# Kernel optimization log

Measured on AMD Instinct MI355X. Metric: run time of the kernel, lower is better.

The kernel has to match this reference:

```python
import jax, jax.numpy as jnp
import numpy as np

NODE_IN, EDGE_IN, HID, L = 16, 8, 128, 4
N_NODES, N_EDGES = 50000, 600000
EPS = 1e-5


def setup_inputs() -> dict:
    key = jax.random.key(0)
    ks = jax.random.split(key, 20)
    def lin(k, fan_in, fan_out):
        b = 1.0 / np.sqrt(fan_in)
        kw, kb = jax.random.split(k)
        return (jax.random.uniform(kw, (fan_in, fan_out), jnp.float32, -b, b),
                jax.random.uniform(kb, (fan_out,), jnp.float32, -b, b))
    x = jax.random.normal(ks[0], (N_NODES, NODE_IN), jnp.float32)
    edge_index = jax.random.randint(ks[1], (2, N_EDGES), 0, N_NODES, jnp.int64)
    edge_attr = jax.random.normal(ks[2], (N_EDGES, EDGE_IN), jnp.float32)
    node_w, node_b = lin(ks[3], NODE_IN, HID)
    edge_w, edge_b = lin(ks[4], EDGE_IN, HID)
    lnode_w, lnode_b, ledge_w, ledge_b, adm_w, adm_b = [], [], [], [], [], []
    for l in range(L):
        w, b = lin(ks[5 + 3 * l], HID, HID); lnode_w.append(w); lnode_b.append(b)
        w, b = lin(ks[6 + 3 * l], HID, HID); ledge_w.append(w); ledge_b.append(b)
        w, b = lin(ks[7 + 3 * l], HID, 1); adm_w.append(w); adm_b.append(b)
    return {
        "x": x, "edge_index": edge_index, "edge_attr": edge_attr,
        "node_w": node_w, "node_b": node_b, "edge_w": edge_w, "edge_b": edge_b,
        "lnode_w": jnp.stack(lnode_w), "lnode_b": jnp.stack(lnode_b),
        "ledge_w": jnp.stack(ledge_w), "ledge_b": jnp.stack(ledge_b),
        "adm_w": jnp.stack(adm_w), "adm_b": jnp.stack(adm_b),
        "gamma": jnp.ones((L, HID), jnp.float32),
        "beta": jnp.zeros((L, HID), jnp.float32),
    }


def reference(x, edge_index, edge_attr, node_w, node_b, edge_w, edge_b,
              lnode_w, lnode_b, ledge_w, ledge_b, adm_w, adm_b, gamma, beta):
    N = x.shape[0]
    src, dst = edge_index[0], edge_index[1]
    h = x @ node_w + node_b              # [N, HID]
    ea = edge_attr @ edge_w + edge_b     # [E, HID]
    for l in range(lnode_w.shape[0]):
        hn = h @ lnode_w[l] + lnode_b[l]                         # lin_node
        y_mag = jax.nn.sigmoid(ea @ adm_w[l] + adm_b[l])         # [E, 1] admittance gate
        e = ea @ ledge_w[l] + ledge_b[l]                         # lin_edge
        msg = y_mag * (hn[src] + e)                              # gated message [E, HID]
        agg = jax.ops.segment_sum(msg, dst, num_segments=N)      # scatter-add
        mu = jnp.mean(agg, axis=-1, keepdims=True)
        var = jnp.mean((agg - mu) ** 2, axis=-1, keepdims=True)
        xn = (agg - mu) * jax.lax.rsqrt(var + EPS) * gamma[l] + beta[l]
        h = h + jax.nn.relu(xn)          # dropout is identity in eval mode
    return h
```

## Files before the change

kernel.cpp:

```cpp
#include <hip/hip_runtime.h>
#include <math.h>

#define N_NODES 50000
#define N_EDGES 600000
#define HID 128
#define NLAYERS 4
#define NODE_IN 16
#define EDGE_IN 8
#define LN_EPS 1e-5f
#define SCAN_BLOCKS ((N_NODES + 255) / 256)

typedef short bf16x8 __attribute__((ext_vector_type(8)));
typedef float f32x4 __attribute__((ext_vector_type(4)));

__device__ __forceinline__ float b2f(unsigned short u) {
    union { unsigned int i; float f; } v; v.i = ((unsigned int)u) << 16; return v.f;
}
__device__ __forceinline__ unsigned short f2b(float x) {
    union { float f; unsigned int i; } v; v.f = x;
    unsigned int b = v.i + 0x7FFFu + ((v.i >> 16) & 1u);
    return (unsigned short)(b >> 16);
}

__global__ void detect_i64(const int* ei, int* flag) {
    __shared__ int nz;
    if (threadIdx.x == 0) nz = 0;
    __syncthreads();
    int acc = 0;
    for (int i = threadIdx.x; i < 1024; i += blockDim.x)
        if (ei[2 * i + 1] != 0) acc = 1;
    if (acc) atomicOr(&nz, 1);
    __syncthreads();
    if (threadIdx.x == 0) *flag = (nz == 0) ? 1 : 0;
}

__device__ __forceinline__ int edge_src(const void* ei, int f, int e) {
    if (f) return (int)((const long long*)ei)[e];
    return ((const int*)ei)[e];
}
__device__ __forceinline__ int edge_dst(const void* ei, int f, int e) {
    if (f) return (int)((const long long*)ei)[N_EDGES + e];
    return ((const int*)ei)[N_EDGES + e];
}

__global__ void hist_k(const void* ei, const int* flag, int* cursor) {
    int e = blockIdx.x * blockDim.x + threadIdx.x;
    if (e >= N_EDGES) return;
    int f = *flag;
    atomicAdd(&cursor[edge_dst(ei, f, e)], 1);
}

__global__ void scan1_k(const int* __restrict__ cursor, int* __restrict__ locex,
                        int* __restrict__ partials) {
    __shared__ int sd[256];
    int t = threadIdx.x, i = blockIdx.x * 256 + t;
    int v = (i < N_NODES) ? cursor[i] : 0;
    sd[t] = v;
    __syncthreads();
    for (int off = 1; off < 256; off <<= 1) {
        int x = (t >= off) ? sd[t - off] : 0;
        __syncthreads();
        sd[t] += x;
        __syncthreads();
    }
    if (i < N_NODES) locex[i] = sd[t] - v;
    if (t == 255) partials[blockIdx.x] = sd[255];
}

__global__ void scan2_k(int* partials) {
    __shared__ int sd[256];
    int t = threadIdx.x;
    int v = (t < SCAN_BLOCKS) ? partials[t] : 0;
    sd[t] = v;
    __syncthreads();
    for (int off = 1; off < 256; off <<= 1) {
        int x = (t >= off) ? sd[t - off] : 0;
        __syncthreads();
        sd[t] += x;
        __syncthreads();
    }
    if (t < SCAN_BLOCKS) partials[t] = sd[t] - v;
    if (t == 255) partials[SCAN_BLOCKS] = sd[255];
}

__global__ void scan3_k(int* __restrict__ row_ptr, int* __restrict__ cursor,
                        const int* __restrict__ partials) {
    int i = blockIdx.x * 256 + threadIdx.x;
    if (i < N_NODES) {
        int r = row_ptr[i] + partials[blockIdx.x];
        row_ptr[i] = r;
        cursor[i] = r;
    }
    if (i == N_NODES) row_ptr[N_NODES] = partials[SCAN_BLOCKS];
}

__global__ void place_k(const void* ei, const int* flag, int* cursor,
                        int* sorted_src, int* sorted_eid) {
    int e = blockIdx.x * blockDim.x + threadIdx.x;
    if (e >= N_EDGES) return;
    int f = *flag;
    int s = edge_src(ei, f, e);
    int d = edge_dst(ei, f, e);
    int pos = atomicAdd(&cursor[d], 1);
    sorted_src[pos] = s;
    sorted_eid[pos] = e;
}

__global__ void precomp_all_k(const float* __restrict__ edge_w, const float* __restrict__ edge_b,
                              const float* __restrict__ ledge_w, const float* __restrict__ ledge_b,
                              const float* __restrict__ lnode_b, const float* __restrict__ lnode_w,
                              const float* __restrict__ adm_w, const float* __restrict__ adm_b,
                              float* __restrict__ M, float* __restrict__ cb,
                              float* __restrict__ v, float* __restrict__ cgate,
                              unsigned short* __restrict__ Wt16) {
    int t = blockIdx.x * 256 + threadIdx.x;
    if (t < 4096) {
        int l = t >> 10, k = (t >> 7) & 7, ch = t & 127;
        const float* lw = ledge_w + (size_t)l * HID * HID;
        float a = 0.f;
        for (int j = 0; j < HID; ++j) a += edge_w[k * HID + j] * lw[j * HID + ch];
        M[t] = a;
    } else if (t < 4608) {
        int u = t - 4096;
        int l = u >> 7, ch = u & 127;
        const float* lw = ledge_w + (size_t)l * HID * HID;
        float a = ledge_b[l * HID + ch] + lnode_b[l * HID + ch];
        for (int j = 0; j < HID; ++j) a += edge_b[j] * lw[j * HID + ch];
        cb[u] = a;
    } else if (t < 4640) {
        int u = t - 4608;
        int l = u >> 3, k = u & 7;
        float a = 0.f;
        for (int j = 0; j < HID; ++j) a += edge_w[k * HID + j] * adm_w[l * HID + j];
        v[u] = a;
    } else if (t < 4644) {
        int l = t - 4640;
        float a = adm_b[l];
        for (int j = 0; j < HID; ++j) a += edge_b[j] * adm_w[l * HID + j];
        cgate[l] = a;
    } else if (t >= 4864 && t < 4864 + NLAYERS * HID * HID) {
        int idx = t - 4864;
        int l = idx >> 14, r = idx & 16383, n = r >> 7, k = r & 127;
        Wt16[idx] = f2b(lnode_w[(size_t)l * HID * HID + k * HID + n]);
    }
}

__global__ __launch_bounds__(256) void reorder_k(
    const int* __restrict__ sorted_eid, const float* __restrict__ edge_attr,
    const float* __restrict__ vw, const float* __restrict__ cgate,
    float* __restrict__ ea_sorted, float* __restrict__ y_sorted) {
    __shared__ float sv[36];
    if (threadIdx.x < 32) sv[threadIdx.x] = vw[threadIdx.x];
    else if (threadIdx.x < 36) sv[threadIdx.x] = cgate[threadIdx.x - 32];
    __syncthreads();
    int p = blockIdx.x * 256 + threadIdx.x;
    if (p >= N_EDGES) return;
    int eid = sorted_eid[p];
    float4 a0 = ((const float4*)edge_attr)[(size_t)eid * 2];
    float4 a1 = ((const float4*)edge_attr)[(size_t)eid * 2 + 1];
    ((float4*)ea_sorted)[(size_t)p * 2] = a0;
    ((float4*)ea_sorted)[(size_t)p * 2 + 1] = a1;
#pragma unroll
    for (int l = 0; l < NLAYERS; ++l) {
        const float* vl = &sv[l * 8];
        float t = sv[32 + l];
        t += a0.x * vl[0] + a0.y * vl[1] + a0.z * vl[2] + a0.w * vl[3];
        t += a1.x * vl[4] + a1.y * vl[5] + a1.z * vl[6] + a1.w * vl[7];
        y_sorted[(size_t)l * N_EDGES + p] = 1.0f / (1.0f + __expf(-t));
    }
}

__global__ __launch_bounds__(256) void node_stats_k(
    const int* __restrict__ row_ptr, const float* __restrict__ ea_sorted,
    const float* __restrict__ y_sorted,
    float* __restrict__ agg8, float* __restrict__ sy_arr) {
    int lane = threadIdx.x & 63;
    int n = (blockIdx.x * 256 + threadIdx.x) >> 6;
    int es = lane >> 3, k = lane & 7;
    int ps = row_ptr[n], pe = row_ptr[n + 1];
    float a0 = 0.f, a1 = 0.f, a2 = 0.f, a3 = 0.f;
    float s0 = 0.f, s1 = 0.f, s2 = 0.f, s3 = 0.f;
    for (int p = ps + es; p < pe; p += 8) {
        float ea = ea_sorted[(size_t)p * EDGE_IN + k];
        float y0 = y_sorted[(size_t)0 * N_EDGES + p];
        float y1 = y_sorted[(size_t)1 * N_EDGES + p];
        float y2 = y_sorted[(size_t)2 * N_EDGES + p];
        float y3 = y_sorted[(size_t)3 * N_EDGES + p];
        a0 += y0 * ea; a1 += y1 * ea; a2 += y2 * ea; a3 += y3 * ea;
        s0 += y0; s1 += y1; s2 += y2; s3 += y3;
    }
#pragma unroll
    for (int m = 8; m <= 32; m <<= 1) {
        a0 += __shfl_xor(a0, m, 64); a1 += __shfl_xor(a1, m, 64);
        a2 += __shfl_xor(a2, m, 64); a3 += __shfl_xor(a3, m, 64);
        s0 += __shfl_xor(s0, m, 64); s1 += __shfl_xor(s1, m, 64);
        s2 += __shfl_xor(s2, m, 64); s3 += __shfl_xor(s3, m, 64);
    }
    if (lane < 8) {
        agg8[((size_t)0 * N_NODES + n) * 8 + k] = a0;
        agg8[((size_t)1 * N_NODES + n) * 8 + k] = a1;
        agg8[((size_t)2 * N_NODES + n) * 8 + k] = a2;
        agg8[((size_t)3 * N_NODES + n) * 8 + k] = a3;
    }
    if (lane == 0) {
        sy_arr[(size_t)0 * N_NODES + n] = s0;
        sy_arr[(size_t)1 * N_NODES + n] = s1;
        sy_arr[(size_t)2 * N_NODES + n] = s2;
        sy_arr[(size_t)3 * N_NODES + n] = s3;
    }
}

__global__ void node_encode_k(const float* __restrict__ x, const float* __restrict__ nw,
                              const float* __restrict__ nb,
                              unsigned short* __restrict__ h16) {
    int idx = blockIdx.x * 256 + threadIdx.x;
    if (idx >= N_NODES * HID) return;
    int n = idx >> 7, c = idx & 127;
    float acc = nb[c];
#pragma unroll
    for (int k = 0; k < NODE_IN; ++k) acc += x[n * NODE_IN + k] * nw[k * HID + c];
    h16[idx] = f2b(acc);
}

__global__ __launch_bounds__(256) void gather16_k(
    const int* __restrict__ row_ptr, const int* __restrict__ sorted_src,
    const float* __restrict__ y_l, const unsigned short* __restrict__ h16,
    unsigned int* __restrict__ gh16) {
    int lane = threadIdx.x & 63;
    int n = (blockIdx.x * 256 + threadIdx.x) >> 6;
    int ps = row_ptr[n], pe = row_ptr[n + 1];
    float a0 = 0.f, a1 = 0.f;
    int p = ps;
    for (; p + 7 < pe; p += 8) {
        int s[8];
        float y[8];
        unsigned int v[8];
#pragma unroll
        for (int i = 0; i < 8; ++i) { s[i] = sorted_src[p + i]; y[i] = y_l[p + i]; }
#pragma unroll
        for (int i = 0; i < 8; ++i)
            v[i] = *(const unsigned int*)(h16 + (size_t)s[i] * HID + lane * 2);
#pragma unroll
        for (int i = 0; i < 8; ++i) {
            a0 += y[i] * b2f((unsigned short)v[i]);
            a1 += y[i] * b2f((unsigned short)(v[i] >> 16));
        }
    }
    for (; p + 3 < pe; p += 4) {
        int s[4];
        float y[4];
        unsigned int v[4];
#pragma unroll
        for (int i = 0; i < 4; ++i) { s[i] = sorted_src[p + i]; y[i] = y_l[p + i]; }
#pragma unroll
        for (int i = 0; i < 4; ++i)
            v[i] = *(const unsigned int*)(h16 + (size_t)s[i] * HID + lane * 2);
#pragma unroll
        for (int i = 0; i < 4; ++i) {
            a0 += y[i] * b2f((unsigned short)v[i]);
            a1 += y[i] * b2f((unsigned short)(v[i] >> 16));
        }
    }
    for (; p < pe; ++p) {
        float y = y_l[p];
        unsigned int v = *(const unsigned int*)(h16 + (size_t)sorted_src[p] * HID + lane * 2);
        a0 += y * b2f((unsigned short)v);
        a1 += y * b2f((unsigned short)(v >> 16));
    }
    gh16[(size_t)n * 64 + lane] = ((unsigned int)f2b(a1) << 16) | f2b(a0);
}

__global__ __launch_bounds__(256) void mfma_ln_k(
    const unsigned short* __restrict__ gh16, const unsigned short* __restrict__ Wt16,
    const float* __restrict__ M_l, const float* __restrict__ cb_l,
    const float* __restrict__ agg8_l, const float* __restrict__ sy_l,
    const float* __restrict__ gm, const float* __restrict__ bt,
    unsigned short* __restrict__ h16, float* __restrict__ outF, int last) {
    __shared__ float red[4][16][2];
    const int tid = threadIdx.x;
    const int w = tid >> 6, lane = tid & 63;
    const int g = lane >> 4, c = lane & 15;
    const int nbase = blockIdx.x * 16;
    const int cf0 = w * 2;

    bf16x8 afrag[4];
#pragma unroll
    for (int kc = 0; kc < 4; ++kc)
        afrag[kc] = *(const bf16x8*)(gh16 + (size_t)(nbase + c) * HID + kc * 32 + g * 8);

    f32x4 acc[2];
#pragma unroll
    for (int t = 0; t < 2; ++t) {
        acc[t] = (f32x4){0.f, 0.f, 0.f, 0.f};
        const unsigned short* wp = Wt16 + (size_t)((cf0 + t) * 16 + c) * HID + g * 8;
#pragma unroll
        for (int kc = 0; kc < 4; ++kc) {
            bf16x8 bfrag = *(const bf16x8*)(wp + kc * 32);
            acc[t] = __builtin_amdgcn_mfma_f32_16x16x32_bf16(afrag[kc], bfrag, acc[t], 0, 0, 0);
        }
    }

    float cbv[2], gav[2], bev[2], mv[2][8];
#pragma unroll
    for (int t = 0; t < 2; ++t) {
        int ch = (cf0 + t) * 16 + c;
        cbv[t] = cb_l[ch]; gav[t] = gm[ch]; bev[t] = bt[ch];
#pragma unroll
        for (int k = 0; k < 8; ++k) mv[t][k] = M_l[k * HID + ch];
    }
#pragma unroll
    for (int r = 0; r < 4; ++r) {
        int node = nbase + 4 * g + r;
        float sy = sy_l[node];
        float4 t0 = ((const float4*)agg8_l)[(size_t)node * 2];
        float4 t1 = ((const float4*)agg8_l)[(size_t)node * 2 + 1];
        float a8[8] = {t0.x, t0.y, t0.z, t0.w, t1.x, t1.y, t1.z, t1.w};
#pragma unroll
        for (int t = 0; t < 2; ++t) {
            float v = sy * cbv[t];
#pragma unroll
            for (int k = 0; k < 8; ++k) v += a8[k] * mv[t][k];
            acc[t][r] += v;
        }
    }

    float sx[4], sq[4];
#pragma unroll
    for (int r = 0; r < 4; ++r) {
        sx[r] = acc[0][r] + acc[1][r];
        sq[r] = acc[0][r] * acc[0][r] + acc[1][r] * acc[1][r];
    }
#pragma unroll
    for (int m = 1; m <= 8; m <<= 1) {
#pragma unroll
        for (int r = 0; r < 4; ++r) {
            sx[r] += __shfl_xor(sx[r], m, 64);
            sq[r] += __shfl_xor(sq[r], m, 64);
        }
    }
    if (c == 0) {
#pragma unroll
        for (int r = 0; r < 4; ++r) {
            red[w][4 * g + r][0] = sx[r];
            red[w][4 * g + r][1] = sq[r];
        }
    }
    __syncthreads();

#pragma unroll
    for (int r = 0; r < 4; ++r) {
        int row = 4 * g + r;
        float SX = red[0][row][0] + red[1][row][0] + red[2][row][0] + red[3][row][0];
        float SQ = red[0][row][1] + red[1][row][1] + red[2][row][1] + red[3][row][1];
        float mean = SX * (1.0f / HID);
        float var = SQ * (1.0f / HID) - mean * mean;
        float rstd = rsqrtf(var + LN_EPS);
        int node = nbase + row;
#pragma unroll
        for (int t = 0; t < 2; ++t) {
            int ch = (cf0 + t) * 16 + c;
            size_t idx = (size_t)node * HID + ch;
            float d = acc[t][r] - mean;
            float o = b2f(h16[idx]) + fmaxf(d * rstd * gav[t] + bev[t], 0.f);
            if (last) outF[idx] = o;
            else      h16[idx] = f2b(o);
        }
    }
}

extern "C" void kernel_launch(void* const* d_in, const int* in_sizes, int n_in,
                              void* d_out, int out_size, void* d_ws, size_t ws_size,
                              hipStream_t stream) {
    const float* x         = (const float*)d_in[0];
    const void*  ei        = d_in[1];
    const float* edge_attr = (const float*)d_in[2];
    const float* node_w    = (const float*)d_in[3];
    const float* node_b    = (const float*)d_in[4];
    const float* edge_w    = (const float*)d_in[5];
    const float* edge_b    = (const float*)d_in[6];
    const float* lnode_w   = (const float*)d_in[7];
    const float* lnode_b   = (const float*)d_in[8];
    const float* ledge_w   = (const float*)d_in[9];
    const float* ledge_b   = (const float*)d_in[10];
    const float* adm_w     = (const float*)d_in[11];
    const float* adm_b     = (const float*)d_in[12];
    const float* gamma     = (const float*)d_in[13];
    const float* beta      = (const float*)d_in[14];
    float* h = (float*)d_out;

    char* wp = (char*)d_ws;
    auto alloc = [&](size_t bytes) -> void* {
        void* p = (void*)wp;
        wp += (bytes + 255) & ~(size_t)255;
        return p;
    };
    int*            flag       = (int*)alloc(256);
    int*            cursor     = (int*)alloc(sizeof(int) * N_NODES);
    int*            row_ptr    = (int*)alloc(sizeof(int) * (N_NODES + 1));
    int*            partials   = (int*)alloc(sizeof(int) * (SCAN_BLOCKS + 1));
    int*            sorted_src = (int*)alloc(sizeof(int) * N_EDGES);
    int*            sorted_eid = (int*)alloc(sizeof(int) * N_EDGES);
    float*          ea_sorted  = (float*)alloc(sizeof(float) * (size_t)N_EDGES * EDGE_IN);
    float*          y_sorted   = (float*)alloc(sizeof(float) * NLAYERS * N_EDGES);
    float*          agg8       = (float*)alloc(sizeof(float) * NLAYERS * N_NODES * 8);
    float*          sy_arr     = (float*)alloc(sizeof(float) * NLAYERS * N_NODES);
    float*          Mw         = (float*)alloc(sizeof(float) * NLAYERS * 8 * HID);
    float*          cbw        = (float*)alloc(sizeof(float) * NLAYERS * HID);
    float*          vw         = (float*)alloc(sizeof(float) * NLAYERS * 8);
    float*          cgate      = (float*)alloc(sizeof(float) * NLAYERS);
    unsigned short* h16        = (unsigned short*)alloc(sizeof(short) * (size_t)N_NODES * HID);
    unsigned short* gh16       = (unsigned short*)alloc(sizeof(short) * (size_t)N_NODES * HID);
    unsigned short* Wt16       = (unsigned short*)alloc(sizeof(short) * NLAYERS * HID * HID);
    (void)ws_size; (void)in_sizes; (void)n_in; (void)out_size;

    hipMemsetAsync(cursor, 0, sizeof(int) * N_NODES, stream);
    detect_i64<<<1, 256, 0, stream>>>((const int*)ei, flag);
    hist_k<<<(N_EDGES + 255) / 256, 256, 0, stream>>>(ei, flag, cursor);
    scan1_k<<<SCAN_BLOCKS, 256, 0, stream>>>(cursor, row_ptr, partials);
    scan2_k<<<1, 256, 0, stream>>>(partials);
    scan3_k<<<SCAN_BLOCKS, 256, 0, stream>>>(row_ptr, cursor, partials);
    place_k<<<(N_EDGES + 255) / 256, 256, 0, stream>>>(ei, flag, cursor, sorted_src, sorted_eid);
    precomp_all_k<<<(4864 + NLAYERS * HID * HID + 255) / 256, 256, 0, stream>>>(
        edge_w, edge_b, ledge_w, ledge_b, lnode_b, lnode_w, adm_w, adm_b,
        Mw, cbw, vw, cgate, Wt16);
    reorder_k<<<(N_EDGES + 255) / 256, 256, 0, stream>>>(sorted_eid, edge_attr,
                                                         vw, cgate, ea_sorted, y_sorted);
    node_stats_k<<<N_NODES / 4, 256, 0, stream>>>(row_ptr, ea_sorted, y_sorted,
                                                  agg8, sy_arr);
    node_encode_k<<<(N_NODES * HID + 255) / 256, 256, 0, stream>>>(x, node_w, node_b, h16);

    for (int l = 0; l < NLAYERS; ++l) {
        gather16_k<<<N_NODES / 4, 256, 0, stream>>>(
            row_ptr, sorted_src, y_sorted + (size_t)l * N_EDGES, h16, (unsigned int*)gh16);
        mfma_ln_k<<<N_NODES / 16, 256, 0, stream>>>(
            gh16, Wt16 + (size_t)l * HID * HID,
            Mw + (size_t)l * 8 * HID, cbw + (size_t)l * HID,
            agg8 + (size_t)l * N_NODES * 8, sy_arr + (size_t)l * N_NODES,
            gamma + (size_t)l * HID, beta + (size_t)l * HID,
            h16, h, (l == NLAYERS - 1) ? 1 : 0);
    }
}
```

Before: 377.8 us.

## Fuse neighbor gather with MFMA layernorm per layer, ping-pong node buffers

Merges the per-layer gather kernel and the MFMA+LayerNorm kernel into one 512-thread kernel. Each block gathers 16 node rows into shared memory and then runs the 128x128 bf16 MFMA and LayerNorm on them, so the gh16 intermediate no longer makes a round trip through global memory. Because the whole layer now reads h while writing the new h, two h buffers are swapped between layers. Node encoding is folded into the precompute kernel to drop one launch. The cost is that gather and MFMA phases no longer overlap across kernels, and each block now does 8 gathers with a barrier before compute.

```diff
diff --git a/kernel.cpp b/kernel.cpp
--- a/kernel.cpp
+++ b/kernel.cpp
@@ -9,6 +9,8 @@
 #define EDGE_IN 8
 #define LN_EPS 1e-5f
 #define SCAN_BLOCKS ((N_NODES + 255) / 256)
+#define ENC_BASE (4864 + NLAYERS * HID * HID)
+#define PRE_TOTAL (ENC_BASE + N_NODES * HID)
 
 typedef short bf16x8 __attribute__((ext_vector_type(8)));
 typedef float f32x4 __attribute__((ext_vector_type(4)));
@@ -110,9 +112,12 @@
                               const float* __restrict__ ledge_w, const float* __restrict__ ledge_b,
                               const float* __restrict__ lnode_b, const float* __restrict__ lnode_w,
                               const float* __restrict__ adm_w, const float* __restrict__ adm_b,
+                              const float* __restrict__ x, const float* __restrict__ node_w,
+                              const float* __restrict__ node_b,
                               float* __restrict__ M, float* __restrict__ cb,
                               float* __restrict__ v, float* __restrict__ cgate,
-                              unsigned short* __restrict__ Wt16) {
+                              unsigned short* __restrict__ Wt16,
+                              unsigned short* __restrict__ h16) {
     int t = blockIdx.x * 256 + threadIdx.x;
     if (t < 4096) {
         int l = t >> 10, k = (t >> 7) & 7, ch = t & 127;
@@ -138,10 +143,17 @@
         float a = adm_b[l];
         for (int j = 0; j < HID; ++j) a += edge_b[j] * adm_w[l * HID + j];
         cgate[l] = a;
-    } else if (t >= 4864 && t < 4864 + NLAYERS * HID * HID) {
+    } else if (t >= 4864 && t < ENC_BASE) {
         int idx = t - 4864;
         int l = idx >> 14, r = idx & 16383, n = r >> 7, k = r & 127;
         Wt16[idx] = f2b(lnode_w[(size_t)l * HID * HID + k * HID + n]);
+    } else if (t >= ENC_BASE && t < PRE_TOTAL) {
+        int idx = t - ENC_BASE;
+        int n = idx >> 7, c = idx & 127;
+        float acc = node_b[c];
+#pragma unroll
+        for (int k = 0; k < NODE_IN; ++k) acc += x[n * NODE_IN + k] * node_w[k * HID + c];
+        h16[idx] = f2b(acc);
     }
 }
 
@@ -210,126 +222,107 @@
     }
 }
 
-__global__ void node_encode_k(const float* __restrict__ x, const float* __restrict__ nw,
-                              const float* __restrict__ nb,
-                              unsigned short* __restrict__ h16) {
-    int idx = blockIdx.x * 256 + threadIdx.x;
-    if (idx >= N_NODES * HID) return;
-    int n = idx >> 7, c = idx & 127;
-    float acc = nb[c];
-#pragma unroll
-    for (int k = 0; k < NODE_IN; ++k) acc += x[n * NODE_IN + k] * nw[k * HID + c];
-    h16[idx] = f2b(acc);
-}
-
-__global__ __launch_bounds__(256) void gather16_k(
+__global__ __launch_bounds__(512, 4) void layer_fused_k(
     const int* __restrict__ row_ptr, const int* __restrict__ sorted_src,
-    const float* __restrict__ y_l, const unsigned short* __restrict__ h16,
-    unsigned int* __restrict__ gh16) {
-    int lane = threadIdx.x & 63;
-    int n = (blockIdx.x * 256 + threadIdx.x) >> 6;
-    int ps = row_ptr[n], pe = row_ptr[n + 1];
-    float a0 = 0.f, a1 = 0.f;
-    int p = ps;
-    for (; p + 7 < pe; p += 8) {
-        int s[8];
-        float y[8];
-        unsigned int v[8];
-#pragma unroll
-        for (int i = 0; i < 8; ++i) { s[i] = sorted_src[p + i]; y[i] = y_l[p + i]; }
-#pragma unroll
-        for (int i = 0; i < 8; ++i)
-            v[i] = *(const unsigned int*)(h16 + (size_t)s[i] * HID + lane * 2);
-#pragma unroll
-        for (int i = 0; i < 8; ++i) {
-            a0 += y[i] * b2f((unsigned short)v[i]);
-            a1 += y[i] * b2f((unsigned short)(v[i] >> 16));
-        }
-    }
-    for (; p + 3 < pe; p += 4) {
-        int s[4];
-        float y[4];
-        unsigned int v[4];
-#pragma unroll
-        for (int i = 0; i < 4; ++i) { s[i] = sorted_src[p + i]; y[i] = y_l[p + i]; }
-#pragma unroll
-        for (int i = 0; i < 4; ++i)
-            v[i] = *(const unsigned int*)(h16 + (size_t)s[i] * HID + lane * 2);
-#pragma unroll
-        for (int i = 0; i < 4; ++i) {
-            a0 += y[i] * b2f((unsigned short)v[i]);
-            a1 += y[i] * b2f((unsigned short)(v[i] >> 16));
-        }
-    }
-    for (; p < pe; ++p) {
-        float y = y_l[p];
-        unsigned int v = *(const unsigned int*)(h16 + (size_t)sorted_src[p] * HID + lane * 2);
-        a0 += y * b2f((unsigned short)v);
-        a1 += y * b2f((unsigned short)(v >> 16));
-    }
-    gh16[(size_t)n * 64 + lane] = ((unsigned int)f2b(a1) << 16) | f2b(a0);
-}
-
-__global__ __launch_bounds__(256) void mfma_ln_k(
-    const unsigned short* __restrict__ gh16, const unsigned short* __restrict__ Wt16,
+    const float* __restrict__ y_l, const unsigned short* __restrict__ Wt16,
     const float* __restrict__ M_l, const float* __restrict__ cb_l,
     const float* __restrict__ agg8_l, const float* __restrict__ sy_l,
     const float* __restrict__ gm, const float* __restrict__ bt,
-    unsigned short* __restrict__ h16, float* __restrict__ outF, int last) {
-    __shared__ float red[4][16][2];
-    const int tid = threadIdx.x;
-    const int w = tid >> 6, lane = tid & 63;
+    const unsigned short* __restrict__ h16_in, unsigned short* __restrict__ h16_out,
+    float* __restrict__ outF, int last) {
+    __shared__ unsigned int ghs[16 * 66];
+    __shared__ float red[8][16][2];
+    const int wid = threadIdx.x >> 6, lane = threadIdx.x & 63;
+    const int nbase = blockIdx.x * 16;
+
+#pragma unroll 1
+    for (int i = 0; i < 2; ++i) {
+        int row = wid * 2 + i;
+        int n = nbase + row;
+        int ps = row_ptr[n], pe = row_ptr[n + 1];
+        float a0 = 0.f, a1 = 0.f;
+        int p = ps;
+        for (; p + 7 < pe; p += 8) {
+            int s[8];
+            float y[8];
+            unsigned int v[8];
+#pragma unroll
+            for (int j = 0; j < 8; ++j) { s[j] = sorted_src[p + j]; y[j] = y_l[p + j]; }
+#pragma unroll
+            for (int j = 0; j < 8; ++j)
+                v[j] = *(const unsigned int*)(h16_in + (size_t)s[j] * HID + lane * 2);
+#pragma unroll
+            for (int j = 0; j < 8; ++j) {
+                a0 += y[j] * b2f((unsigned short)v[j]);
+                a1 += y[j] * b2f((unsigned short)(v[j] >> 16));
+            }
+        }
+        for (; p + 3 < pe; p += 4) {
+            int s[4];
+            float y[4];
+            unsigned int v[4];
+#pragma unroll
+            for (int j = 0; j < 4; ++j) { s[j] = sorted_src[p + j]; y[j] = y_l[p + j]; }
+#pragma unroll
+            for (int j = 0; j < 4; ++j)
+                v[j] = *(const unsigned int*)(h16_in + (size_t)s[j] * HID + lane * 2);
+#pragma unroll
+            for (int j = 0; j < 4; ++j) {
+                a0 += y[j] * b2f((unsigned short)v[j]);
+                a1 += y[j] * b2f((unsigned short)(v[j] >> 16));
+            }
+        }
+        for (; p < pe; ++p) {
+            float y = y_l[p];
+            unsigned int v = *(const unsigned int*)(h16_in + (size_t)sorted_src[p] * HID + lane * 2);
+            a0 += y * b2f((unsigned short)v);
+            a1 += y * b2f((unsigned short)(v >> 16));
+        }
+        ghs[row * 66 + lane] = ((unsigned int)f2b(a1) << 16) | f2b(a0);
+    }
+    __syncthreads();
+
     const int g = lane >> 4, c = lane & 15;
-    const int nbase = blockIdx.x * 16;
-    const int cf0 = w * 2;
-
+    const int cf = wid;
     bf16x8 afrag[4];
 #pragma unroll
-    for (int kc = 0; kc < 4; ++kc)
-        afrag[kc] = *(const bf16x8*)(gh16 + (size_t)(nbase + c) * HID + kc * 32 + g * 8);
-
-    f32x4 acc[2];
-#pragma unroll
-    for (int t = 0; t < 2; ++t) {
-        acc[t] = (f32x4){0.f, 0.f, 0.f, 0.f};
-        const unsigned short* wp = Wt16 + (size_t)((cf0 + t) * 16 + c) * HID + g * 8;
+    for (int kc = 0; kc < 4; ++kc) {
+        union { unsigned int q[4]; bf16x8 v; } u;
+        int base = c * 66 + kc * 16 + g * 4;
+#pragma unroll
+        for (int j = 0; j < 4; ++j) u.q[j] = ghs[base + j];
+        afrag[kc] = u.v;
+    }
+    f32x4 acc = (f32x4){0.f, 0.f, 0.f, 0.f};
+    {
+        const unsigned short* wp = Wt16 + (size_t)(cf * 16 + c) * HID + g * 8;
 #pragma unroll
         for (int kc = 0; kc < 4; ++kc) {
             bf16x8 bfrag = *(const bf16x8*)(wp + kc * 32);
-            acc[t] = __builtin_amdgcn_mfma_f32_16x16x32_bf16(afrag[kc], bfrag, acc[t], 0, 0, 0);
-        }
-    }
-
-    float cbv[2], gav[2], bev[2], mv[2][8];
-#pragma unroll
-    for (int t = 0; t < 2; ++t) {
-        int ch = (cf0 + t) * 16 + c;
-        cbv[t] = cb_l[ch]; gav[t] = gm[ch]; bev[t] = bt[ch];
-#pragma unroll
-        for (int k = 0; k < 8; ++k) mv[t][k] = M_l[k * HID + ch];
-    }
+            acc = __builtin_amdgcn_mfma_f32_16x16x32_bf16(afrag[kc], bfrag, acc, 0, 0, 0);
+        }
+    }
+
+    const int ch = cf * 16 + c;
+    float cbv = cb_l[ch], gav = gm[ch], bev = bt[ch];
+    float mv[8];
+#pragma unroll
+    for (int k = 0; k < 8; ++k) mv[k] = M_l[k * HID + ch];
 #pragma unroll
     for (int r = 0; r < 4; ++r) {
         int node = nbase + 4 * g + r;
         float sy = sy_l[node];
         float4 t0 = ((const float4*)agg8_l)[(size_t)node * 2];
         float4 t1 = ((const float4*)agg8_l)[(size_t)node * 2 + 1];
-        float a8[8] = {t0.x, t0.y, t0.z, t0.w, t1.x, t1.y, t1.z, t1.w};
-#pragma unroll
-        for (int t = 0; t < 2; ++t) {
-            float v = sy * cbv[t];
-#pragma unroll
-            for (int k = 0; k < 8; ++k) v += a8[k] * mv[t][k];
-            acc[t][r] += v;
-        }
+        float vv = sy * cbv;
+        vv += t0.x * mv[0] + t0.y * mv[1] + t0.z * mv[2] + t0.w * mv[3];
+        vv += t1.x * mv[4] + t1.y * mv[5] + t1.z * mv[6] + t1.w * mv[7];
+        acc[r] += vv;
     }
 
     float sx[4], sq[4];
 #pragma unroll
-    for (int r = 0; r < 4; ++r) {
-        sx[r] = acc[0][r] + acc[1][r];
-        sq[r] = acc[0][r] * acc[0][r] + acc[1][r] * acc[1][r];
-    }
+    for (int r = 0; r < 4; ++r) { sx[r] = acc[r]; sq[r] = acc[r] * acc[r]; }
 #pragma unroll
     for (int m = 1; m <= 8; m <<= 1) {
 #pragma unroll
@@ -341,8 +334,8 @@
     if (c == 0) {
 #pragma unroll
         for (int r = 0; r < 4; ++r) {
-            red[w][4 * g + r][0] = sx[r];
-            red[w][4 * g + r][1] = sq[r];
+            red[wid][4 * g + r][0] = sx[r];
+            red[wid][4 * g + r][1] = sq[r];
         }
     }
     __syncthreads();
@@ -350,21 +343,18 @@
 #pragma unroll
     for (int r = 0; r < 4; ++r) {
         int row = 4 * g + r;
-        float SX = red[0][row][0] + red[1][row][0] + red[2][row][0] + red[3][row][0];
-        float SQ = red[0][row][1] + red[1][row][1] + red[2][row][1] + red[3][row][1];
+        float SX = 0.f, SQ = 0.f;
+#pragma unroll
+        for (int w2 = 0; w2 < 8; ++w2) { SX += red[w2][row][0]; SQ += red[w2][row][1]; }
         float mean = SX * (1.0f / HID);
         float var = SQ * (1.0f / HID) - mean * mean;
         float rstd = rsqrtf(var + LN_EPS);
         int node = nbase + row;
-#pragma unroll
-        for (int t = 0; t < 2; ++t) {
-            int ch = (cf0 + t) * 16 + c;
-            size_t idx = (size_t)node * HID + ch;
-            float d = acc[t][r] - mean;
-            float o = b2f(h16[idx]) + fmaxf(d * rstd * gav[t] + bev[t], 0.f);
-            if (last) outF[idx] = o;
-            else      h16[idx] = f2b(o);
-        }
+        size_t idx = (size_t)node * HID + ch;
+        float d = acc[r] - mean;
+        float o = b2f(h16_in[idx]) + fmaxf(d * rstd * gav + bev, 0.f);
+        if (last) outF[idx] = o;
+        else      h16_out[idx] = f2b(o);
     }
 }
 
@@ -408,8 +398,8 @@
     float*          cbw        = (float*)alloc(sizeof(float) * NLAYERS * HID);
     float*          vw         = (float*)alloc(sizeof(float) * NLAYERS * 8);
     float*          cgate      = (float*)alloc(sizeof(float) * NLAYERS);
-    unsigned short* h16        = (unsigned short*)alloc(sizeof(short) * (size_t)N_NODES * HID);
-    unsigned short* gh16       = (unsigned short*)alloc(sizeof(short) * (size_t)N_NODES * HID);
+    unsigned short* h16a       = (unsigned short*)alloc(sizeof(short) * (size_t)N_NODES * HID);
+    unsigned short* h16b       = (unsigned short*)alloc(sizeof(short) * (size_t)N_NODES * HID);
     unsigned short* Wt16       = (unsigned short*)alloc(sizeof(short) * NLAYERS * HID * HID);
     (void)ws_size; (void)in_sizes; (void)n_in; (void)out_size;
 
@@ -420,23 +410,24 @@
     scan2_k<<<1, 256, 0, stream>>>(partials);
     scan3_k<<<SCAN_BLOCKS, 256, 0, stream>>>(row_ptr, cursor, partials);
     place_k<<<(N_EDGES + 255) / 256, 256, 0, stream>>>(ei, flag, cursor, sorted_src, sorted_eid);
-    precomp_all_k<<<(4864 + NLAYERS * HID * HID + 255) / 256, 256, 0, stream>>>(
+    precomp_all_k<<<(PRE_TOTAL + 255) / 256, 256, 0, stream>>>(
         edge_w, edge_b, ledge_w, ledge_b, lnode_b, lnode_w, adm_w, adm_b,
-        Mw, cbw, vw, cgate, Wt16);
+        x, node_w, node_b, Mw, cbw, vw, cgate, Wt16, h16a);
     reorder_k<<<(N_EDGES + 255) / 256, 256, 0, stream>>>(sorted_eid, edge_attr,
                                                          vw, cgate, ea_sorted, y_sorted);
     node_stats_k<<<N_NODES / 4, 256, 0, stream>>>(row_ptr, ea_sorted, y_sorted,
                                                   agg8, sy_arr);
-    node_encode_k<<<(N_NODES * HID + 255) / 256, 256, 0, stream>>>(x, node_w, node_b, h16);
-
+
+    unsigned short* hin = h16a;
+    unsigned short* hout = h16b;
     for (int l = 0; l < NLAYERS; ++l) {
-        gather16_k<<<N_NODES / 4, 256, 0, stream>>>(
-            row_ptr, sorted_src, y_sorted + (size_t)l * N_EDGES, h16, (unsigned int*)gh16);
-        mfma_ln_k<<<N_NODES / 16, 256, 0, stream>>>(
-            gh16, Wt16 + (size_t)l * HID * HID,
+        layer_fused_k<<<N_NODES / 16, 512, 0, stream>>>(
+            row_ptr, sorted_src, y_sorted + (size_t)l * N_EDGES,
+            Wt16 + (size_t)l * HID * HID,
             Mw + (size_t)l * 8 * HID, cbw + (size_t)l * HID,
             agg8 + (size_t)l * N_NODES * 8, sy_arr + (size_t)l * N_NODES,
             gamma + (size_t)l * HID, beta + (size_t)l * HID,
-            h16, h, (l == NLAYERS - 1) ? 1 : 0);
-    }
-}
+            hin, hout, h, (l == NLAYERS - 1) ? 1 : 0);
+        unsigned short* t = hin; hin = hout; hout = t;
+    }
+}
```

Result: faster. 356.7 us, median of 3 (-5.6%).
